# Kernel optimization log

Hardware: AMD Instinct MI355X
Metric: run time of the kernel (lower is better)

The kernel has to match this reference:

```python
import jax, jax.numpy as jnp
import numpy as np

H = 100  # hidden size of both LSTM layers (fixed in the module)

def lstm_layer(x, w_ih, w_hh, b_ih, b_hh):
    # x: [B, T, I]; w_ih: [4H, I]; w_hh: [4H, H]; biases: [4H]
    # PyTorch gate order: input, forget, cell(g), output.
    B, T, _ = x.shape
    xg = jnp.einsum('bti,gi->btg', x, w_ih) + b_ih + b_hh  # [B, T, 4H], input GEMM hoisted out of the scan
    h0 = jnp.zeros((B, H), x.dtype)
    c0 = jnp.zeros((B, H), x.dtype)
    w_hh_t = w_hh.T  # [H, 4H]

    def step(carry, xg_t):
        h, c = carry
        g = xg_t + h @ w_hh_t                # [B, 4H]
        i, f, gg, o = jnp.split(g, 4, axis=-1)
        i = jax.nn.sigmoid(i)
        f = jax.nn.sigmoid(f)
        gg = jnp.tanh(gg)
        o = jax.nn.sigmoid(o)
        c = f * c + i * gg
        h = o * jnp.tanh(c)
        return (h, c), h

    _, hs = jax.lax.scan(step, (h0, c0), jnp.swapaxes(xg, 0, 1))  # hs: [T, B, H]
    return jnp.swapaxes(hs, 0, 1)  # [B, T, H]


def setup_inputs() -> dict:
    key = jax.random.key(0)
    ks = jax.random.split(key, 13)
    B, T, I = 256, 2048, 8
    s = lambda fan: 1.0 / np.sqrt(fan)
    u = lambda k, shape, fan: jax.random.uniform(k, shape, jnp.float32, -s(fan), s(fan))
    return {
        'x': jax.random.normal(ks[0], (B, T, I), jnp.float32),
        'w_ih1': u(ks[1], (4 * H, I), H), 'w_hh1': u(ks[2], (4 * H, H), H),
        'b_ih1': u(ks[3], (4 * H,), H), 'b_hh1': u(ks[4], (4 * H,), H),
        'w_ih2': u(ks[5], (4 * H, H), H), 'w_hh2': u(ks[6], (4 * H, H), H),
        'b_ih2': u(ks[7], (4 * H,), H), 'b_hh2': u(ks[8], (4 * H,), H),
        'fc1_w': u(ks[9], (25, H), H), 'fc1_b': u(ks[10], (25,), H),
        'fc2_w': u(ks[11], (1, 25), 25), 'fc2_b': u(ks[12], (1,), 25),
    }


def reference(x, w_ih1, w_hh1, b_ih1, b_hh1, w_ih2, w_hh2, b_ih2, b_hh2,
              fc1_w, fc1_b, fc2_w, fc2_b):
    # Dropout layers are identity in eval mode.
    h1 = lstm_layer(x, w_ih1, w_hh1, b_ih1, b_hh1)    # [B, T, H]
    h2 = lstm_layer(h1, w_ih2, w_hh2, b_ih2, b_hh2)   # [B, T, H]
    last = h2[:, -1, :]                               # [B, H]
    y = last @ fc1_w.T + fc1_b                        # [B, 25]
    return y @ fc2_w.T + fc2_b                        # [B, 1]
```

## Files before the change

### kernel.cpp

```cpp
#include <hip/hip_runtime.h>

#define BB 256
#define TT 2048
#define HD 100

typedef _Float16 h2v __attribute__((ext_vector_type(2)));
typedef _Float16 f16x8 __attribute__((ext_vector_type(8)));
typedef float f32x4 __attribute__((ext_vector_type(4)));

__device__ __forceinline__ float fdot2(unsigned w, unsigned h, float c) {
#if __has_builtin(__builtin_amdgcn_fdot2)
    return __builtin_amdgcn_fdot2(__builtin_bit_cast(h2v, w),
                                  __builtin_bit_cast(h2v, h), c, false);
#else
    h2v a = __builtin_bit_cast(h2v, w), b = __builtin_bit_cast(h2v, h);
    c = fmaf((float)a[0], (float)b[0], c);
    c = fmaf((float)a[1], (float)b[1], c);
    return c;
#endif
}
__device__ __forceinline__ unsigned packh2(float a, float b) {
    h2v p; p[0] = (_Float16)a; p[1] = (_Float16)b;
    return __builtin_bit_cast(unsigned, p);
}
__device__ __forceinline__ float rcp_f(float x) {
#if __has_builtin(__builtin_amdgcn_rcpf)
    return __builtin_amdgcn_rcpf(x);
#else
    return 1.0f / x;
#endif
}
__device__ __forceinline__ float sigmoid_f(float x) { return rcp_f(1.0f + __expf(-x)); }
__device__ __forceinline__ float tanh_f(float x) {
    return fmaf(2.0f, rcp_f(1.0f + __expf(-2.0f * x)), -1.0f);
}
__device__ __forceinline__ f32x4 mfma16(uint4 a, uint4 b, f32x4 c) {
    return __builtin_amdgcn_mfma_f32_16x16x32_f16(
        __builtin_bit_cast(f16x8, a), __builtin_bit_cast(f16x8, b), c, 0, 0, 0);
}

__global__ __launch_bounds__(256, 1) void lstm_rec(
    const float* __restrict__ x,
    const float* __restrict__ w_ih1, const float* __restrict__ w_hh1,
    const float* __restrict__ b_ih1, const float* __restrict__ b_hh1,
    const float* __restrict__ w_hh2,
    const float* __restrict__ xg2,
    unsigned* __restrict__ h1buf,
    float* __restrict__ c1s,
    unsigned* __restrict__ h2sp,
    float* __restrict__ c2s,
    float* __restrict__ h2f,
    int Tc, int ch, int nch)
{
    const int role = blockIdx.x >> 8;
    const int b    = blockIdx.x & 255;
    const int tid  = threadIdx.x, lane = tid & 63;

    __shared__ unsigned hsp[64];
    __shared__ float glds[400];
    __shared__ unsigned xs[2][32][4];
    __shared__ float XG[2][8][400];

    const bool isG = tid < 200;
    const int  gt  = isG ? tid : 199;
    const int  um  = tid >> 2;
    const bool isU = ((tid & 3) == 3) && (tid < 200);
    const int  g0 = 2 * gt, g1r = 2 * gt + 1;
    const bool tg = (gt >= 100) && (gt < 150);

    if (role == 0) {
        if (ch >= nch) return;
        const int t0 = ch * Tc, first = (ch == 0);
        const bool isX = ((tid & 3) == 1) && (tid < 128);

        unsigned wA[54], wB[54];
        float bias0, bias1, cc0 = 0.f, cc1 = 0.f;
        { const float4* p = (const float4*)(w_ih1 + (size_t)g0 * 8);
          float4 v0 = p[0], v1 = p[1];
          wA[0] = packh2(v0.x, v0.y); wA[1] = packh2(v0.z, v0.w);
          wA[2] = packh2(v1.x, v1.y); wA[3] = packh2(v1.z, v1.w); }
        { const float4* p = (const float4*)(w_ih1 + (size_t)g1r * 8);
          float4 v0 = p[0], v1 = p[1];
          wB[0] = packh2(v0.x, v0.y); wB[1] = packh2(v0.z, v0.w);
          wB[2] = packh2(v1.x, v1.y); wB[3] = packh2(v1.z, v1.w); }
        { const float4* p = (const float4*)(w_hh1 + (size_t)g0 * HD);
          #pragma unroll
          for (int q = 0; q < 25; ++q) { float4 v = p[q];
              wA[4 + 2*q] = packh2(v.x, v.y); wA[5 + 2*q] = packh2(v.z, v.w); } }
        { const float4* p = (const float4*)(w_hh1 + (size_t)g1r * HD);
          #pragma unroll
          for (int q = 0; q < 25; ++q) { float4 v = p[q];
              wB[4 + 2*q] = packh2(v.x, v.y); wB[5 + 2*q] = packh2(v.z, v.w); } }
        bias0 = b_ih1[g0] + b_hh1[g0];
        bias1 = b_ih1[g1r] + b_hh1[g1r];

        if (isU && !first) {
            cc0 = c1s[b * HD + 2 * um];
            cc1 = c1s[b * HD + 2 * um + 1];
        }
        if (tid < 64) {
            unsigned v = 0u;
            if (!first && tid < 50)
                v = h1buf[((size_t)(Tc - 1) * BB + b) * 52 + tid];
            hsp[tid] = v;
        }
        if (isX) {
            const int s = um;
            const float4* p = (const float4*)(x + ((size_t)b * TT + t0 + s) * 8);
            float4 v0 = p[0], v1 = p[1];
            xs[0][s][0] = packh2(v0.x, v0.y); xs[0][s][1] = packh2(v0.z, v0.w);
            xs[0][s][2] = packh2(v1.x, v1.y); xs[0][s][3] = packh2(v1.z, v1.w);
        }
        __syncthreads();

        float4 pa = {0,0,0,0}, pb = {0,0,0,0};
        #pragma unroll 1
        for (int t = 0; t < Tc; ++t) {
            const bool pf = ((t & 31) == 0) && (t + 32 < Tc) && isX;
            if (pf) {
                const float4* p = (const float4*)(x + ((size_t)b * TT + t0 + t + 32 + um) * 8);
                pa = p[0]; pb = p[1];
            }
            const unsigned st = hsp[lane];
            const unsigned* xq = xs[(t >> 5) & 1][t & 31];
            unsigned x0 = xq[0], x1 = xq[1], x2 = xq[2], x3 = xq[3];
            float a0 = bias0, a1 = bias1, a2 = 0.f, a3 = 0.f;
            a0 = fdot2(wA[0], x0, a0); a1 = fdot2(wB[0], x0, a1);
            a2 = fdot2(wA[1], x1, a2); a3 = fdot2(wB[1], x1, a3);
            a0 = fdot2(wA[2], x2, a0); a1 = fdot2(wB[2], x2, a1);
            a2 = fdot2(wA[3], x3, a2); a3 = fdot2(wB[3], x3, a3);
            #pragma unroll
            for (int k = 0; k < 50; ++k) {
                unsigned hk = (unsigned)__builtin_amdgcn_readlane((int)st, k);
                if (k & 1) { a2 = fdot2(wA[4 + k], hk, a2); a3 = fdot2(wB[4 + k], hk, a3); }
                else       { a0 = fdot2(wA[4 + k], hk, a0); a1 = fdot2(wB[4 + k], hk, a1); }
            }
            float r0 = a0 + a2, r1 = a1 + a3;
            r0 = tg ? tanh_f(r0) : sigmoid_f(r0);
            r1 = tg ? tanh_f(r1) : sigmoid_f(r1);
            if (isG) *(float2*)(glds + 2 * tid) = make_float2(r0, r1);
            __syncthreads();
            if (isU) {
                const int j = 2 * um;
                float2 gi = *(const float2*)(glds + j);
                float2 gf = *(const float2*)(glds + 100 + j);
                float2 gg = *(const float2*)(glds + 200 + j);
                float2 go = *(const float2*)(glds + 300 + j);
                cc0 = gf.x * cc0 + gi.x * gg.x;
                cc1 = gf.y * cc1 + gi.y * gg.y;
                float h0 = go.x * tanh_f(cc0);
                float h1v = go.y * tanh_f(cc1);
                unsigned hp = packh2(h0, h1v);
                hsp[um] = hp;
                h1buf[((size_t)t * BB + b) * 52 + um] = hp;
                if (t == Tc - 1) { c1s[b * HD + j] = cc0; c1s[b * HD + j + 1] = cc1; }
            }
            if (pf) {
                const int nb2 = ((t >> 5) + 1) & 1; const int s = um;
                xs[nb2][s][0] = packh2(pa.x, pa.y); xs[nb2][s][1] = packh2(pa.z, pa.w);
                xs[nb2][s][2] = packh2(pb.x, pb.y); xs[nb2][s][3] = packh2(pb.z, pb.w);
            }
            __syncthreads();
        }
    } else {
        if (ch < 1) return;
        const int first = (ch == 1), last = (ch == nch);

        unsigned wHA[50], wHB[50];
        float cc0 = 0.f, cc1 = 0.f;
        { const float4* p = (const float4*)(w_hh2 + (size_t)g0 * HD);
          #pragma unroll
          for (int q = 0; q < 25; ++q) { float4 v = p[q];
              wHA[2*q] = packh2(v.x, v.y); wHA[2*q+1] = packh2(v.z, v.w); } }
        { const float4* p = (const float4*)(w_hh2 + (size_t)g1r * HD);
          #pragma unroll
          for (int q = 0; q < 25; ++q) { float4 v = p[q];
              wHB[2*q] = packh2(v.x, v.y); wHB[2*q+1] = packh2(v.z, v.w); } }

        if (isU && !first) {
            cc0 = c2s[b * HD + 2 * um];
            cc1 = c2s[b * HD + 2 * um + 1];
        }
        if (tid < 64) {
            unsigned v = 0u;
            if (!first && tid < 50) v = h2sp[b * 50 + tid];
            hsp[tid] = v;
        }
        #pragma unroll
        for (int j = 0; j < 4; ++j) {
            const int idx = tid + j * 256;
            if (idx < 800) {
                const int s = idx / 100, n4 = idx - s * 100;
                *(float4*)&XG[0][s][n4 * 4] =
                    *(const float4*)&xg2[(((size_t)s * BB) + b) * 400 + n4 * 4];
            }
        }
        __syncthreads();

        float4 pre[4];
        #pragma unroll 1
        for (int t = 0; t < Tc; ++t) {
            const int g = t >> 3;
            const bool pfg = ((t & 7) == 0) && ((g + 1) * 8 < Tc);
            if (pfg) {
                #pragma unroll
                for (int j = 0; j < 4; ++j) {
                    const int idx = tid + j * 256;
                    if (idx < 800) {
                        const int s = idx / 100, n4 = idx - s * 100;
                        pre[j] = *(const float4*)
                            &xg2[(((size_t)((g + 1) * 8 + s) * BB) + b) * 400 + n4 * 4];
                    }
                }
            }
            const unsigned st2 = hsp[lane];
            const float2 xg = *(const float2*)&XG[g & 1][t & 7][2 * gt];
            float a0 = xg.x, a1 = xg.y, a2 = 0.f, a3 = 0.f;
            #pragma unroll
            for (int k = 0; k < 50; ++k) {
                unsigned hk = (unsigned)__builtin_amdgcn_readlane((int)st2, k);
                if (k & 1) { a2 = fdot2(wHA[k], hk, a2); a3 = fdot2(wHB[k], hk, a3); }
                else       { a0 = fdot2(wHA[k], hk, a0); a1 = fdot2(wHB[k], hk, a1); }
            }
            float r0 = a0 + a2, r1 = a1 + a3;
            r0 = tg ? tanh_f(r0) : sigmoid_f(r0);
            r1 = tg ? tanh_f(r1) : sigmoid_f(r1);
            if (isG) *(float2*)(glds + 2 * tid) = make_float2(r0, r1);
            __syncthreads();
            if ((t & 7) == 4 && ((g + 1) * 8 < Tc)) {
                #pragma unroll
                for (int j = 0; j < 4; ++j) {
                    const int idx = tid + j * 256;
                    if (idx < 800) {
                        const int s = idx / 100, n4 = idx - s * 100;
                        *(float4*)&XG[(g + 1) & 1][s][n4 * 4] = pre[j];
                    }
                }
            }
            if (isU) {
                const int j = 2 * um;
                float2 gi = *(const float2*)(glds + j);
                float2 gf = *(const float2*)(glds + 100 + j);
                float2 gg = *(const float2*)(glds + 200 + j);
                float2 go = *(const float2*)(glds + 300 + j);
                cc0 = gf.x * cc0 + gi.x * gg.x;
                cc1 = gf.y * cc1 + gi.y * gg.y;
                float h0 = go.x * tanh_f(cc0);
                float h1v = go.y * tanh_f(cc1);
                hsp[um] = packh2(h0, h1v);
                if (t == Tc - 1) {
                    h2sp[b * 50 + um] = packh2(h0, h1v);
                    c2s[b * HD + j] = cc0; c2s[b * HD + j + 1] = cc1;
                    if (last) { h2f[b * HD + j] = h0; h2f[b * HD + j + 1] = h1v; }
                }
            }
            __syncthreads();
        }
    }
}

__global__ __launch_bounds__(256, 1) void xg2_gemm(
    const unsigned* __restrict__ h1buf,
    const float* __restrict__ w_ih2,
    const float* __restrict__ b_ih2, const float* __restrict__ b_hh2,
    float* __restrict__ xg2,
    int Mrows)
{
    const int tid = threadIdx.x, lane = tid & 63, w = tid >> 6;
    const int W  = blockIdx.x * 4 + w;
    const int mt = W / 25, nt = W - mt * 25;
    if (mt * 16 >= Mrows) return;
    const int col = lane & 15, kg = lane >> 4;
    const int r    = mt * 16 + col;
    const int gate = nt * 16 + col;

    uint4 a[4];
    #pragma unroll
    for (int kt = 0; kt < 4; ++kt)
        a[kt] = *(const uint4*)&h1buf[(size_t)r * 52 + kt * 16 + kg * 4];

    uint4 bf[4];
    #pragma unroll
    for (int kt = 0; kt < 3; ++kt) {
        const float4 va = *(const float4*)&w_ih2[(size_t)gate * HD + kt * 32 + kg * 8];
        const float4 vb = *(const float4*)&w_ih2[(size_t)gate * HD + kt * 32 + kg * 8 + 4];
        bf[kt] = make_uint4(packh2(va.x, va.y), packh2(va.z, va.w),
                            packh2(vb.x, vb.y), packh2(vb.z, vb.w));
    }
    {
        if (kg == 0) {
            const float4 va = *(const float4*)&w_ih2[(size_t)gate * HD + 96];
            bf[3] = make_uint4(packh2(va.x, va.y), packh2(va.z, va.w), 0u, 0u);
        } else {
            bf[3] = make_uint4(0u, 0u, 0u, 0u);
        }
    }

    f32x4 acc = {0.f, 0.f, 0.f, 0.f};
    #pragma unroll
    for (int kt = 0; kt < 4; ++kt) acc = mfma16(a[kt], bf[kt], acc);

    const float bias = b_ih2[gate] + b_hh2[gate];
    #pragma unroll
    for (int j = 0; j < 4; ++j)
        xg2[((size_t)mt * 16 + kg * 4 + j) * 400 + gate] = acc[j] + bias;
}

__global__ void fc_head(const float* __restrict__ h2,
                        const float* __restrict__ fc1_w, const float* __restrict__ fc1_b,
                        const float* __restrict__ fc2_w, const float* __restrict__ fc2_b,
                        float* __restrict__ out)
{
    const int bidx = threadIdx.x;
    const float* h = h2 + (size_t)bidx * HD;
    float hv[HD];
    #pragma unroll
    for (int kk = 0; kk < HD / 4; ++kk) {
        float4 v = *(const float4*)(h + 4 * kk);
        hv[4*kk+0] = v.x; hv[4*kk+1] = v.y; hv[4*kk+2] = v.z; hv[4*kk+3] = v.w;
    }
    float y = fc2_b[0];
    #pragma unroll
    for (int m = 0; m < 25; ++m) {
        float a = fc1_b[m];
        const float* wp = fc1_w + m * HD;
        #pragma unroll
        for (int k = 0; k < HD; ++k) a += hv[k] * wp[k];
        y += a * fc2_w[m];
    }
    out[bidx] = y;
}

extern "C" void kernel_launch(void* const* d_in, const int* in_sizes, int n_in,
                              void* d_out, int out_size, void* d_ws, size_t ws_size,
                              hipStream_t stream) {
    const float* x     = (const float*)d_in[0];
    const float* w_ih1 = (const float*)d_in[1];
    const float* w_hh1 = (const float*)d_in[2];
    const float* b_ih1 = (const float*)d_in[3];
    const float* b_hh1 = (const float*)d_in[4];
    const float* w_ih2 = (const float*)d_in[5];
    const float* w_hh2 = (const float*)d_in[6];
    const float* b_ih2 = (const float*)d_in[7];
    const float* b_hh2 = (const float*)d_in[8];
    const float* fc1_w = (const float*)d_in[9];
    const float* fc1_b = (const float*)d_in[10];
    const float* fc2_w = (const float*)d_in[11];
    const float* fc2_b = (const float*)d_in[12];
    float* out = (float*)d_out;

    int Tc = 128;
    auto need = [](int tc) -> size_t {
        return (size_t)tc * BB * 400 * 4
             + ((size_t)tc * BB * 52 + 64) * 4
             + (size_t)BB * (HD * 3 + 50) * 4;
    };
    while (Tc > 16 && need(Tc) > ws_size) Tc >>= 1;
    const int nch = TT / Tc;
    const int Mrows = Tc * BB;

    float* xg2 = (float*)d_ws;
    unsigned* h1buf = (unsigned*)(xg2 + (size_t)Mrows * 400);
    float* c1s = (float*)(h1buf + (size_t)Mrows * 52 + 64);
    float* c2s = c1s + (size_t)BB * HD;
    float* h2f = c2s + (size_t)BB * HD;
    unsigned* h2sp = (unsigned*)(h2f + (size_t)BB * HD);

    const int gblocks = (Mrows / 16) * 25 / 4;

    for (int ch = 0; ch < nch; ++ch) {
        lstm_rec<<<512, 256, 0, stream>>>(x, w_ih1, w_hh1, b_ih1, b_hh1, w_hh2,
                                          xg2, h1buf, c1s, h2sp, c2s, h2f,
                                          Tc, ch, nch);
        xg2_gemm<<<gblocks, 256, 0, stream>>>(h1buf, w_ih2, b_ih2, b_hh2,
                                              xg2, Mrows);
    }
    lstm_rec<<<512, 256, 0, stream>>>(x, w_ih1, w_hh1, b_ih1, b_hh1, w_hh2,
                                      xg2, h1buf, c1s, h2sp, c2s, h2f,
                                      Tc, nch, nch);
    fc_head<<<1, 256, 0, stream>>>(h2f, fc1_w, fc1_b, fc2_w, fc2_b, out);
}
```

Measured before the change: 3.186 ms.

## Remove second barrier per LSTM step via double-buffered gates and redundant cell update

Every wave now computes the cell/hidden update redundantly for 50 lanes and keeps h in a register, so the shared hidden-state buffer and the second __syncthreads per timestep go away. The gate buffer is double-buffered by timestep parity. In the layer-1 role, h1 history is staged in a small LDS ring and flushed to global memory in batches of 8 steps instead of one scattered store per step. This shortens the serial per-step critical path at the cost of duplicated transcendental work in every wave and a shared-memory arena with manual offsets.

```diff
diff --git a/kernel.cpp b/kernel.cpp
--- a/kernel.cpp
+++ b/kernel.cpp
@@ -7,6 +7,11 @@
 typedef _Float16 h2v __attribute__((ext_vector_type(2)));
 typedef _Float16 f16x8 __attribute__((ext_vector_type(8)));
 typedef float f32x4 __attribute__((ext_vector_type(4)));
+
+#define OFF_XS  3200
+#define OFF_H1R 4224
+#define OFF_XG  3200
+#define ARENA   28800
 
 __device__ __forceinline__ float fdot2(unsigned w, unsigned h, float c) {
 #if __has_builtin(__builtin_amdgcn_fdot2)
@@ -54,27 +59,27 @@
 {
     const int role = blockIdx.x >> 8;
     const int b    = blockIdx.x & 255;
-    const int tid  = threadIdx.x, lane = tid & 63;
-
-    __shared__ unsigned hsp[64];
-    __shared__ float glds[400];
-    __shared__ unsigned xs[2][32][4];
-    __shared__ float XG[2][8][400];
+    const int tid  = threadIdx.x, lane = tid & 63, w = tid >> 6;
+
+    __shared__ __align__(16) char LB[ARENA];
+    float* glds = (float*)LB;
 
     const bool isG = tid < 200;
     const int  gt  = isG ? tid : 199;
-    const int  um  = tid >> 2;
-    const bool isU = ((tid & 3) == 3) && (tid < 200);
     const int  g0 = 2 * gt, g1r = 2 * gt + 1;
     const bool tg = (gt >= 100) && (gt < 150);
+    const int  lidx = (lane < 50) ? lane : 49;
 
     if (role == 0) {
         if (ch >= nch) return;
         const int t0 = ch * Tc, first = (ch == 0);
+        unsigned* xs  = (unsigned*)(LB + OFF_XS);
+        unsigned* H1R = (unsigned*)(LB + OFF_H1R);
         const bool isX = ((tid & 3) == 1) && (tid < 128);
+        const int  um  = tid >> 2;
 
         unsigned wA[54], wB[54];
-        float bias0, bias1, cc0 = 0.f, cc1 = 0.f;
+        float bias0, bias1;
         { const float4* p = (const float4*)(w_ih1 + (size_t)g0 * 8);
           float4 v0 = p[0], v1 = p[1];
           wA[0] = packh2(v0.x, v0.y); wA[1] = packh2(v0.z, v0.w);
@@ -94,35 +99,32 @@
         bias0 = b_ih1[g0] + b_hh1[g0];
         bias1 = b_ih1[g1r] + b_hh1[g1r];
 
-        if (isU && !first) {
-            cc0 = c1s[b * HD + 2 * um];
-            cc1 = c1s[b * HD + 2 * um + 1];
-        }
-        if (tid < 64) {
-            unsigned v = 0u;
-            if (!first && tid < 50)
-                v = h1buf[((size_t)(Tc - 1) * BB + b) * 52 + tid];
-            hsp[tid] = v;
-        }
+        float cc0 = 0.f, cc1 = 0.f;
+        unsigned hreg = 0u;
+        if (!first) {
+            hreg = h1buf[((size_t)(Tc - 1) * BB + b) * 52 + lidx];
+            if (lane < 50) {
+                cc0 = c1s[b * HD + 2 * lane];
+                cc1 = c1s[b * HD + 2 * lane + 1];
+            }
+        } 
         if (isX) {
             const int s = um;
-            const float4* p = (const float4*)(x + ((size_t)b * TT + t0 + s) * 8);
+            const int tt = (t0 + s < TT) ? (t0 + s) : (TT - 1);
+            const float4* p = (const float4*)(x + (size_t)(b * TT + tt) * 8);
             float4 v0 = p[0], v1 = p[1];
-            xs[0][s][0] = packh2(v0.x, v0.y); xs[0][s][1] = packh2(v0.z, v0.w);
-            xs[0][s][2] = packh2(v1.x, v1.y); xs[0][s][3] = packh2(v1.z, v1.w);
+            xs[(0 * 32 + s) * 4 + 0] = packh2(v0.x, v0.y);
+            xs[(0 * 32 + s) * 4 + 1] = packh2(v0.z, v0.w);
+            xs[(0 * 32 + s) * 4 + 2] = packh2(v1.x, v1.y);
+            xs[(0 * 32 + s) * 4 + 3] = packh2(v1.z, v1.w);
         }
         __syncthreads();
 
         float4 pa = {0,0,0,0}, pb = {0,0,0,0};
         #pragma unroll 1
         for (int t = 0; t < Tc; ++t) {
-            const bool pf = ((t & 31) == 0) && (t + 32 < Tc) && isX;
-            if (pf) {
-                const float4* p = (const float4*)(x + ((size_t)b * TT + t0 + t + 32 + um) * 8);
-                pa = p[0]; pb = p[1];
-            }
-            const unsigned st = hsp[lane];
-            const unsigned* xq = xs[(t >> 5) & 1][t & 31];
+            const unsigned st = hreg;
+            const unsigned* xq = xs + (((t >> 5) & 1) * 32 + (t & 31)) * 4;
             unsigned x0 = xq[0], x1 = xq[1], x2 = xq[2], x3 = xq[3];
             float a0 = bias0, a1 = bias1, a2 = 0.f, a3 = 0.f;
             a0 = fdot2(wA[0], x0, a0); a1 = fdot2(wB[0], x0, a1);
@@ -138,36 +140,64 @@
             float r0 = a0 + a2, r1 = a1 + a3;
             r0 = tg ? tanh_f(r0) : sigmoid_f(r0);
             r1 = tg ? tanh_f(r1) : sigmoid_f(r1);
-            if (isG) *(float2*)(glds + 2 * tid) = make_float2(r0, r1);
+            if (isG) *(float2*)(glds + (t & 1) * 400 + 2 * gt) = make_float2(r0, r1);
             __syncthreads();
-            if (isU) {
-                const int j = 2 * um;
-                float2 gi = *(const float2*)(glds + j);
-                float2 gf = *(const float2*)(glds + 100 + j);
-                float2 gg = *(const float2*)(glds + 200 + j);
-                float2 go = *(const float2*)(glds + 300 + j);
-                cc0 = gf.x * cc0 + gi.x * gg.x;
-                cc1 = gf.y * cc1 + gi.y * gg.y;
-                float h0 = go.x * tanh_f(cc0);
-                float h1v = go.y * tanh_f(cc1);
-                unsigned hp = packh2(h0, h1v);
-                hsp[um] = hp;
-                h1buf[((size_t)t * BB + b) * 52 + um] = hp;
-                if (t == Tc - 1) { c1s[b * HD + j] = cc0; c1s[b * HD + j + 1] = cc1; }
-            }
-            if (pf) {
-                const int nb2 = ((t >> 5) + 1) & 1; const int s = um;
-                xs[nb2][s][0] = packh2(pa.x, pa.y); xs[nb2][s][1] = packh2(pa.z, pa.w);
-                xs[nb2][s][2] = packh2(pb.x, pb.y); xs[nb2][s][3] = packh2(pb.z, pb.w);
-            }
-            __syncthreads();
+            if (isX && (t & 31) == 0 && t + 32 < Tc) {
+                const float4* p = (const float4*)(x + (size_t)(b * TT + t0 + t + 32 + um) * 8);
+                pa = p[0]; pb = p[1];
+            }
+            {
+                const float* g = glds + (t & 1) * 400;
+                if (lane < 50) {
+                    float2 gi = *(const float2*)(g + 2 * lane);
+                    float2 gf = *(const float2*)(g + 100 + 2 * lane);
+                    float2 gg = *(const float2*)(g + 200 + 2 * lane);
+                    float2 go = *(const float2*)(g + 300 + 2 * lane);
+                    cc0 = gf.x * cc0 + gi.x * gg.x;
+                    cc1 = gf.y * cc1 + gi.y * gg.y;
+                    float h0  = go.x * tanh_f(cc0);
+                    float h1v = go.y * tanh_f(cc1);
+                    hreg = packh2(h0, h1v);
+                    if (w == 0) {
+                        H1R[(t & 15) * 52 + lane] = hreg;
+                        if (t == Tc - 1) {
+                            c1s[b * HD + 2 * lane]     = cc0;
+                            c1s[b * HD + 2 * lane + 1] = cc1;
+                        }
+                    }
+                }
+            }
+            if (isX && (t & 31) == 16) {
+                const int nb2 = ((t >> 5) + 1) & 1;
+                xs[(nb2 * 32 + um) * 4 + 0] = packh2(pa.x, pa.y);
+                xs[(nb2 * 32 + um) * 4 + 1] = packh2(pa.z, pa.w);
+                xs[(nb2 * 32 + um) * 4 + 2] = packh2(pb.x, pb.y);
+                xs[(nb2 * 32 + um) * 4 + 3] = packh2(pb.z, pb.w);
+            }
+            if ((t & 7) == 3 && t >= 11) {
+                const int s0 = ((t >> 3) - 1) << 3;
+                for (int i = tid; i < 400; i += 256) {
+                    const int j = i / 50, pr = i - j * 50;
+                    h1buf[((size_t)(s0 + j) * BB + b) * 52 + pr] =
+                        H1R[((s0 + j) & 15) * 52 + pr];
+                }
+            }
+        }
+        __syncthreads();
+        {
+            const int s0 = Tc - 8;
+            for (int i = tid; i < 400; i += 256) {
+                const int j = i / 50, pr = i - j * 50;
+                h1buf[((size_t)(s0 + j) * BB + b) * 52 + pr] =
+                    H1R[((s0 + j) & 15) * 52 + pr];
+            }
         }
     } else {
         if (ch < 1) return;
         const int first = (ch == 1), last = (ch == nch);
+        float* XG = (float*)(LB + OFF_XG);
 
         unsigned wHA[50], wHB[50];
-        float cc0 = 0.f, cc1 = 0.f;
         { const float4* p = (const float4*)(w_hh2 + (size_t)g0 * HD);
           #pragma unroll
           for (int q = 0; q < 25; ++q) { float4 v = p[q];
@@ -177,22 +207,22 @@
           for (int q = 0; q < 25; ++q) { float4 v = p[q];
               wHB[2*q] = packh2(v.x, v.y); wHB[2*q+1] = packh2(v.z, v.w); } }
 
-        if (isU && !first) {
-            cc0 = c2s[b * HD + 2 * um];
-            cc1 = c2s[b * HD + 2 * um + 1];
-        }
-        if (tid < 64) {
-            unsigned v = 0u;
-            if (!first && tid < 50) v = h2sp[b * 50 + tid];
-            hsp[tid] = v;
+        float cc0 = 0.f, cc1 = 0.f;
+        unsigned hreg = 0u;
+        if (!first) {
+            hreg = h2sp[b * 50 + lidx];
+            if (lane < 50) {
+                cc0 = c2s[b * HD + 2 * lane];
+                cc1 = c2s[b * HD + 2 * lane + 1];
+            }
         }
         #pragma unroll
         for (int j = 0; j < 4; ++j) {
             const int idx = tid + j * 256;
             if (idx < 800) {
                 const int s = idx / 100, n4 = idx - s * 100;
-                *(float4*)&XG[0][s][n4 * 4] =
-                    *(const float4*)&xg2[(((size_t)s * BB) + b) * 400 + n4 * 4];
+                *(float4*)&XG[(0 * 8 + s) * 400 + n4 * 4] =
+                    *(const float4*)&xg2[((size_t)s * BB + b) * 400 + n4 * 4];
             }
         }
         __syncthreads();
@@ -201,60 +231,64 @@
         #pragma unroll 1
         for (int t = 0; t < Tc; ++t) {
             const int g = t >> 3;
-            const bool pfg = ((t & 7) == 0) && ((g + 1) * 8 < Tc);
-            if (pfg) {
+            const unsigned st = hreg;
+            const float2 xg = *(const float2*)&XG[((g & 1) * 8 + (t & 7)) * 400 + 2 * gt];
+            float a0 = xg.x, a1 = xg.y, a2 = 0.f, a3 = 0.f;
+            #pragma unroll
+            for (int k = 0; k < 50; ++k) {
+                unsigned hk = (unsigned)__builtin_amdgcn_readlane((int)st, k);
+                if (k & 1) { a2 = fdot2(wHA[k], hk, a2); a3 = fdot2(wHB[k], hk, a3); }
+                else       { a0 = fdot2(wHA[k], hk, a0); a1 = fdot2(wHB[k], hk, a1); }
+            }
+            float r0 = a0 + a2, r1 = a1 + a3;
+            r0 = tg ? tanh_f(r0) : sigmoid_f(r0);
+            r1 = tg ? tanh_f(r1) : sigmoid_f(r1);
+            if (isG) *(float2*)(glds + (t & 1) * 400 + 2 * gt) = make_float2(r0, r1);
+            __syncthreads();
+            if ((t & 7) == 0 && (g + 1) * 8 < Tc) {
                 #pragma unroll
                 for (int j = 0; j < 4; ++j) {
                     const int idx = tid + j * 256;
                     if (idx < 800) {
                         const int s = idx / 100, n4 = idx - s * 100;
                         pre[j] = *(const float4*)
-                            &xg2[(((size_t)((g + 1) * 8 + s) * BB) + b) * 400 + n4 * 4];
+                            &xg2[((size_t)((g + 1) * 8 + s) * BB + b) * 400 + n4 * 4];
                     }
                 }
             }
-            const unsigned st2 = hsp[lane];
-            const float2 xg = *(const float2*)&XG[g & 1][t & 7][2 * gt];
-            float a0 = xg.x, a1 = xg.y, a2 = 0.f, a3 = 0.f;
-            #pragma unroll
-            for (int k = 0; k < 50; ++k) {
-                unsigned hk = (unsigned)__builtin_amdgcn_readlane((int)st2, k);
-                if (k & 1) { a2 = fdot2(wHA[k], hk, a2); a3 = fdot2(wHB[k], hk, a3); }
-                else       { a0 = fdot2(wHA[k], hk, a0); a1 = fdot2(wHB[k], hk, a1); }
-            }
-            float r0 = a0 + a2, r1 = a1 + a3;
-            r0 = tg ? tanh_f(r0) : sigmoid_f(r0);
-            r1 = tg ? tanh_f(r1) : sigmoid_f(r1);
-            if (isG) *(float2*)(glds + 2 * tid) = make_float2(r0, r1);
-            __syncthreads();
-            if ((t & 7) == 4 && ((g + 1) * 8 < Tc)) {
+            {
+                const float* gl = glds + (t & 1) * 400;
+                if (lane < 50) {
+                    float2 gi = *(const float2*)(gl + 2 * lane);
+                    float2 gf = *(const float2*)(gl + 100 + 2 * lane);
+                    float2 gg = *(const float2*)(gl + 200 + 2 * lane);
+                    float2 go = *(const float2*)(gl + 300 + 2 * lane);
+                    cc0 = gf.x * cc0 + gi.x * gg.x;
+                    cc1 = gf.y * cc1 + gi.y * gg.y;
+                    float h0  = go.x * tanh_f(cc0);
+                    float h1v = go.y * tanh_f(cc1);
+                    hreg = packh2(h0, h1v);
+                    if (w == 0 && t == Tc - 1) {
+                        h2sp[b * 50 + lane] = hreg;
+                        c2s[b * HD + 2 * lane]     = cc0;
+                        c2s[b * HD + 2 * lane + 1] = cc1;
+                        if (last) {
+                            h2f[b * HD + 2 * lane]     = h0;
+                            h2f[b * HD + 2 * lane + 1] = h1v;
+                        }
+                    }
+                }
+            }
+            if ((t & 7) == 4 && (g + 1) * 8 < Tc) {
                 #pragma unroll
                 for (int j = 0; j < 4; ++j) {
                     const int idx = tid + j * 256;
                     if (idx < 800) {
                         const int s = idx / 100, n4 = idx - s * 100;
-                        *(float4*)&XG[(g + 1) & 1][s][n4 * 4] = pre[j];
+                        *(float4*)&XG[(((g + 1) & 1) * 8 + s) * 400 + n4 * 4] = pre[j];
                     }
                 }
             }
-            if (isU) {
-                const int j = 2 * um;
-                float2 gi = *(const float2*)(glds + j);
-                float2 gf = *(const float2*)(glds + 100 + j);
-                float2 gg = *(const float2*)(glds + 200 + j);
-                float2 go = *(const float2*)(glds + 300 + j);
-                cc0 = gf.x * cc0 + gi.x * gg.x;
-                cc1 = gf.y * cc1 + gi.y * gg.y;
-                float h0 = go.x * tanh_f(cc0);
-                float h1v = go.y * tanh_f(cc1);
-                hsp[um] = packh2(h0, h1v);
-                if (t == Tc - 1) {
-                    h2sp[b * 50 + um] = packh2(h0, h1v);
-                    c2s[b * HD + j] = cc0; c2s[b * HD + j + 1] = cc1;
-                    if (last) { h2f[b * HD + j] = h0; h2f[b * HD + j + 1] = h1v; }
-                }
-            }
-            __syncthreads();
         }
     }
 }
@@ -287,13 +321,11 @@
         bf[kt] = make_uint4(packh2(va.x, va.y), packh2(va.z, va.w),
                             packh2(vb.x, vb.y), packh2(vb.z, vb.w));
     }
-    {
-        if (kg == 0) {
-            const float4 va = *(const float4*)&w_ih2[(size_t)gate * HD + 96];
-            bf[3] = make_uint4(packh2(va.x, va.y), packh2(va.z, va.w), 0u, 0u);
-        } else {
-            bf[3] = make_uint4(0u, 0u, 0u, 0u);
-        }
+    if (kg == 0) {
+        const float4 va = *(const float4*)&w_ih2[(size_t)gate * HD + 96];
+        bf[3] = make_uint4(packh2(va.x, va.y), packh2(va.z, va.w), 0u, 0u);
+    } else {
+        bf[3] = make_uint4(0u, 0u, 0u, 0u);
     }
 
     f32x4 acc = {0.f, 0.f, 0.f, 0.f};
```

New measurement: 3.078 ms. 1.04x faster.
